# Kernel tuning notes

Hardware: AMD Instinct MI355X
Metric: run time of the kernel (lower is better)

## Reference

```python
import jax, jax.numpy as jnp
import numpy as np

SR = 22050
FMIN = 220.0
N_BINS = 84
BPO = 12
HOP = 512
NORM_P = 1
T_SAMPLES = 8388608  # 2**23 samples of audio


def _make_kernels():
    Q = 1.0 / (2.0 ** (1.0 / BPO) - 1.0)
    fftLen = 2 ** int(np.ceil(np.log2(np.ceil(Q * SR / FMIN))))  # 2048
    freqs = FMIN * 2.0 ** (np.arange(N_BINS) / float(BPO))
    temp = np.zeros((N_BINS, fftLen), dtype=np.complex64)
    for k in range(N_BINS):
        freq = freqs[k]
        l = np.ceil(Q * SR / freq)
        if l % 2 == 1:
            start = int(np.ceil(fftLen / 2.0 - l / 2.0)) - 1
        else:
            start = int(np.ceil(fftLen / 2.0 - l / 2.0))
        li = int(l)
        n = np.arange(li)
        hann = 0.5 - 0.5 * np.cos(2 * np.pi * n / li)  # periodic ('fftbins=True') hann
        idx = np.arange(np.floor(-l / 2.0), np.floor(l / 2.0))
        temp[k, start:start + li] = hann * np.exp(1j * 2 * np.pi * freq / SR * idx) / li
    spec = np.fft.fft(temp, axis=1)[:, : fftLen // 2 + 1]
    kr = spec.real.astype(np.float32)
    ki = spec.imag.astype(np.float32)
    # norm=1 branch: divide by L1 norm (over bins axis, dim=0) of complex magnitude
    mag = np.sqrt(kr ** 2 + ki ** 2)
    denom = np.sum(np.abs(mag), axis=0)  # shape [freq_bins]
    kr = (kr / denom).astype(np.float32)
    ki = (ki / denom).astype(np.float32)
    # Fourier kernels: freq_scale='no', windowing='no'
    freq_bins = fftLen // 2 + 1
    s = np.arange(fftLen, dtype=np.float64)
    kk = np.arange(freq_bins, dtype=np.float64)
    ang = 2 * np.pi * np.outer(kk, s) / fftLen  # [freq_bins, fftLen]
    wsin = np.sin(ang).astype(np.float32)
    wcos = np.cos(ang).astype(np.float32)
    return kr, ki, wcos, wsin


def setup_inputs() -> dict:
    key = jax.random.key(0)
    x = jax.random.normal(key, (T_SAMPLES,), dtype=jnp.float32)
    kr, ki, wcos, wsin = _make_kernels()
    return {
        "x": x,
        "wcos": jnp.asarray(wcos),
        "wsin": jnp.asarray(wsin),
        "kr": jnp.asarray(kr),
        "ki": jnp.asarray(ki),
    }


def reference(x, wcos, wsin, kr, ki):
    fftLen = wcos.shape[1]  # 2048
    n_frames = (x.shape[0] - fftLen) // HOP + 1  # static under jit
    # frame the signal: equivalent to conv1d(x, w, stride=HOP) with kernels w
    idx = jnp.arange(n_frames)[:, None] * HOP + jnp.arange(fftLen)[None, :]
    frames = x[idx]  # [n_frames, fftLen]
    fourier_real = jnp.einsum("fn,kn->kf", frames, wcos)  # [freq_bins, n_frames]
    fourier_imag = jnp.einsum("fn,kn->kf", frames, wsin)
    cqt_real = kr @ fourier_real - ki @ fourier_imag  # [n_bins, n_frames]
    cqt_imag = kr @ fourier_imag + ki @ fourier_real
    cqt = jnp.sqrt(cqt_real ** 2 + cqt_imag ** 2)
    return cqt[None]  # [1, n_bins, n_frames]
```

## Files before the change

### kernel.cpp

```cpp
#include <hip/hip_runtime.h>


#define HOPS 512
#define NBINS 84
#define FREQB 1025
#define NFRAMES 16381
#define TSAMP 8388608
#define SPAN 34304
#define XLSZ 34572
#define KP16 138

typedef short bf16x8 __attribute__((ext_vector_type(8)));
typedef float f32x16 __attribute__((ext_vector_type(16)));

union B8 { struct { ushort4 lo, hi; } p; bf16x8 v; uint4 u; };

__device__ __forceinline__ unsigned short f32_to_bf16(float f) {
    union { float f; unsigned u; } v; v.f = f;
    return (unsigned short)((v.u + 0x7FFFu + ((v.u >> 16) & 1u)) >> 16);
}
__device__ __forceinline__ unsigned pk_bf16(float lo, float hi) {
    return (unsigned)f32_to_bf16(lo) | ((unsigned)f32_to_bf16(hi) << 16);
}
__device__ __forceinline__ bf16x8 pack8(const float* s) {
    B8 r;
    r.u.x = pk_bf16(s[0], s[1]); r.u.y = pk_bf16(s[2], s[3]);
    r.u.z = pk_bf16(s[4], s[5]); r.u.w = pk_bf16(s[6], s[7]);
    return r.v;
}

__device__ __forceinline__ float cos_rev(float r) { return __builtin_amdgcn_cosf(r); }
__device__ __forceinline__ float sin_rev(float r) { return __builtin_amdgcn_sinf(r); }

__global__ __launch_bounds__(64) void aprep_kernel(
    const float* __restrict__ kr, const float* __restrict__ ki,
    unsigned short* __restrict__ Apf)
{
    const int bid = blockIdx.x;
    const int mt = bid / KP16, k16 = bid % KP16;
    const int l = threadIdx.x;
    const int c32 = l & 31, h = l >> 5;
    const int row = mt * 32 + c32;
    const int b = row >> 1, im = row & 1;
    const bool bok = b < NBINS;
    const float* cosp = (im ? ki : kr) + (size_t)(bok ? b : 0) * FREQB;
    const float* sinp = (im ? kr : ki) + (size_t)(bok ? b : 0) * FREQB;
    const float ssign = im ? 1.f : -1.f;

    unsigned short o[8];
    #pragma unroll
    for (int j = 0; j < 8; ++j) {
        int k = k16 * 16 + h * 8 + j;
        float v = 0.f;
        if (bok) {
            if (k <= 1024)       v = cosp[k];
            else if (k <= 2049)  v = ssign * sinp[k - 1025];
        }
        o[j] = f32_to_bf16(v);
    }
    uint4 pk;
    pk.x = (unsigned)o[0] | ((unsigned)o[1] << 16);
    pk.y = (unsigned)o[2] | ((unsigned)o[3] << 16);
    pk.z = (unsigned)o[4] | ((unsigned)o[5] << 16);
    pk.w = (unsigned)o[6] | ((unsigned)o[7] << 16);
    *(uint4*)(Apf + (size_t)bid * 512 + (size_t)l * 8) = pk;
}

__global__ __launch_bounds__(256) void wfused_kernel(
    const unsigned short* __restrict__ Apf, unsigned short* __restrict__ Wpf)
{
    __shared__ float4 red[3][4][64];

    const int bid = blockIdx.x;
    const int mt = bid >> 6, nt = bid & 63;
    const int t = threadIdx.x;
    const int w = t >> 6, l = t & 63;
    const int c32 = l & 31, h = l >> 5;
    const int n = nt * 32 + c32;

    f32x16 acc;
    #pragma unroll
    for (int i = 0; i < 16; ++i) acc[i] = 0.f;

    const int k0 = w * 33;
    const int kcnt = (w < 3) ? 33 : 30;
    const unsigned short* ap = Apf + (size_t)(mt * KP16 + k0) * 512 + (size_t)l * 8;

    for (int i = 0; i < kcnt; ++i) {
        const int k16 = k0 + i;
        B8 bf; bf.u = *(const uint4*)(ap + (size_t)i * 512);
        float tv[8];
        const int kb = k16 * 16 + h * 8;
        if (k16 <= 63) {
            #pragma unroll
            for (int j = 0; j < 8; ++j) {
                int p = __mul24(kb + j, n) & 2047;
                tv[j] = cos_rev((float)p * (1.f / 2048.f));
            }
        } else if (k16 >= 65 && k16 <= 127) {
            #pragma unroll
            for (int j = 0; j < 8; ++j) {
                int p = __mul24(kb + j - 1025, n) & 2047;
                tv[j] = sin_rev((float)p * (1.f / 2048.f));
            }
        } else {
            #pragma unroll
            for (int j = 0; j < 8; ++j) {
                int k = kb + j;
                float v = 0.f;
                if (k <= 1024) {
                    int p = __mul24(k, n) & 2047;
                    v = cos_rev((float)p * (1.f / 2048.f));
                } else if (k <= 2049) {
                    int p = __mul24(k - 1025, n) & 2047;
                    v = sin_rev((float)p * (1.f / 2048.f));
                }
                tv[j] = v;
            }
        }
        acc = __builtin_amdgcn_mfma_f32_32x32x16_bf16(pack8(tv), bf.v, acc, 0, 0, 0);
    }

    if (w > 0) {
        #pragma unroll
        for (int q = 0; q < 4; ++q)
            red[w - 1][q][l] = make_float4(acc[4*q+0], acc[4*q+1], acc[4*q+2], acc[4*q+3]);
    }
    __syncthreads();
    if (w == 0) {
        #pragma unroll
        for (int s = 0; s < 3; ++s) {
            #pragma unroll
            for (int q = 0; q < 4; ++q) {
                float4 v = red[s][q][l];
                acc[4*q+0] += v.x; acc[4*q+1] += v.y;
                acc[4*q+2] += v.z; acc[4*q+3] += v.w;
            }
        }
        #pragma unroll
        for (int g = 0; g < 4; ++g) {
            uint2 qo;
            qo.x = pk_bf16(acc[4*g+0], acc[4*g+1]);
            qo.y = pk_bf16(acc[4*g+2], acc[4*g+3]);
            size_t off = (size_t)(mt * 128 + nt * 2 + (g >> 1)) * 512
                       + (size_t)(c32 + 32 * (g & 1)) * 8 + 4 * h;
            *(uint2*)(Wpf + off) = qo;
        }
    }
}

__global__ __launch_bounds__(768) void cqt_kernel(
    const float* __restrict__ x, const unsigned short* __restrict__ Wpf,
    float* __restrict__ out)
{
    __shared__ __align__(16) unsigned short xl[XLSZ];

    const int t = threadIdx.x;
    const int f0 = blockIdx.x * 64;
    const long S0 = (long)f0 * HOPS;
    const int valid = (int)((TSAMP - S0) < (long)SPAN ? (TSAMP - S0) : (long)SPAN);

    #pragma unroll
    for (int i = 0; i < 12; ++i) {
        int idx4 = t + i * 768;
        if (idx4 < 8576) {
            int s = idx4 * 4;
            float4 v = make_float4(0.f, 0.f, 0.f, 0.f);
            if (s + 4 <= valid) v = *(const float4*)(x + S0 + s);
            ushort4 o;
            o.x = f32_to_bf16(v.x); o.y = f32_to_bf16(v.y);
            o.z = f32_to_bf16(v.z); o.w = f32_to_bf16(v.w);
            *(ushort4*)(&xl[s + 4 * (s >> 9)]) = o;
        }
    }
    __syncthreads();

    const int w = t >> 6, l = t & 63;
    const int mg = w >> 1, fg = w & 1;
    const int c32 = l & 31, h = l >> 5;

    const unsigned short* apf = Wpf + (size_t)mg * (128 * 512) + l * 8;
    const int sbase = (fg * 32 + c32) * HOPS + h * 8;

    f32x16 acc;
    #pragma unroll
    for (int i = 0; i < 16; ++i) acc[i] = 0.f;

    auto ldsB = [&](int k16) -> bf16x8 {
        int s = sbase + k16 * 16;
        int off = s + 4 * (s >> 9);
        B8 r;
        r.p.lo = *(const ushort4*)(&xl[off]);
        r.p.hi = *(const ushort4*)(&xl[off + 4]);
        return r.v;
    };

    uint4 Abuf[2][8];
    #pragma unroll
    for (int j = 0; j < 8; ++j)
        Abuf[0][j] = *(const uint4*)(apf + (size_t)j * 512);

    #pragma unroll
    for (int c = 0; c < 16; ++c) {
        const int cur = c & 1, nxt = cur ^ 1;
        if (c < 15) {
            #pragma unroll
            for (int j = 0; j < 8; ++j)
                Abuf[nxt][j] = *(const uint4*)(apf + (size_t)((c + 1) * 8 + j) * 512);
        }
        #pragma unroll
        for (int j = 0; j < 8; ++j) {
            B8 af; af.u = Abuf[cur][j];
            acc = __builtin_amdgcn_mfma_f32_32x32x16_bf16(af.v, ldsB(c * 8 + j), acc, 0, 0, 0);
        }
    }

    const int f = f0 + fg * 32 + c32;
    if (f < NFRAMES) {
        #pragma unroll
        for (int rp = 0; rp < 4; ++rp) {
            int base = mg * 32 + 8 * rp + 4 * h;
            int b0 = base >> 1;
            float r0 = acc[4 * rp + 0], i0 = acc[4 * rp + 1];
            float r1 = acc[4 * rp + 2], i1 = acc[4 * rp + 3];
            if (b0 < NBINS)
                out[(size_t)b0 * NFRAMES + f] = sqrtf(r0 * r0 + i0 * i0);
            if (b0 + 1 < NBINS)
                out[(size_t)(b0 + 1) * NFRAMES + f] = sqrtf(r1 * r1 + i1 * i1);
        }
    }
}

extern "C" void kernel_launch(void* const* d_in, const int* in_sizes, int n_in,
                              void* d_out, int out_size, void* d_ws, size_t ws_size,
                              hipStream_t stream) {
    const float* x    = (const float*)d_in[0];
    const float* kr   = (const float*)d_in[3];
    const float* ki   = (const float*)d_in[4];
    float* out = (float*)d_out;

    unsigned short* Wpf = (unsigned short*)d_ws;
    unsigned short* Apf = (unsigned short*)((char*)d_ws + 786432);

    aprep_kernel<<<dim3(6 * KP16), dim3(64), 0, stream>>>(kr, ki, Apf);
    wfused_kernel<<<dim3(384), dim3(256), 0, stream>>>(Apf, Wpf);
    cqt_kernel<<<dim3(256), dim3(768), 0, stream>>>(x, Wpf, out);
}
```

Baseline: 118.2 us.

## Halve cqt block tile to 32 frames, raise occupancy, add nontemporal IO and setprio

The cqt kernel now gives each block 32 frames and 6 waves (one per M-tile) instead of 64 frames and 12 waves. This doubles the grid to 512 blocks so all CUs get work, and halves LDS per block so 3 blocks can share a CU. Input loads and output stores become nontemporal, and the MFMA loop runs at raised wave priority. In exchange, each block re-stages more overlapping audio per frame, and every block reads the full W matrix, doubling total W traffic from L2.

New measurement: 124.4 us. 5.2% more time.

```diff
diff --git a/kernel.cpp b/kernel.cpp
--- a/kernel.cpp
+++ b/kernel.cpp
@@ -6,12 +6,13 @@
 #define FREQB 1025
 #define NFRAMES 16381
 #define TSAMP 8388608
-#define SPAN 34304
-#define XLSZ 34572
+#define SPAN32 17920
+#define XL32 18060
 #define KP16 138
 
 typedef short bf16x8 __attribute__((ext_vector_type(8)));
 typedef float f32x16 __attribute__((ext_vector_type(16)));
+typedef float f32x4 __attribute__((ext_vector_type(4)));
 
 union B8 { struct { ushort4 lo, hi; } p; bf16x8 v; uint4 u; };
 
@@ -149,24 +150,25 @@
     }
 }
 
-__global__ __launch_bounds__(768) void cqt_kernel(
+__global__ __launch_bounds__(384, 3) void cqt_kernel(
     const float* __restrict__ x, const unsigned short* __restrict__ Wpf,
     float* __restrict__ out)
 {
-    __shared__ __align__(16) unsigned short xl[XLSZ];
+    __shared__ __align__(16) unsigned short xl[XL32];
 
     const int t = threadIdx.x;
-    const int f0 = blockIdx.x * 64;
+    const int f0 = blockIdx.x * 32;
     const long S0 = (long)f0 * HOPS;
-    const int valid = (int)((TSAMP - S0) < (long)SPAN ? (TSAMP - S0) : (long)SPAN);
+    const int valid = (int)((TSAMP - S0) < (long)SPAN32 ? (TSAMP - S0) : (long)SPAN32);
 
     #pragma unroll
     for (int i = 0; i < 12; ++i) {
-        int idx4 = t + i * 768;
-        if (idx4 < 8576) {
+        int idx4 = t + i * 384;
+        if (idx4 < 4480) {
             int s = idx4 * 4;
-            float4 v = make_float4(0.f, 0.f, 0.f, 0.f);
-            if (s + 4 <= valid) v = *(const float4*)(x + S0 + s);
+            f32x4 v = {0.f, 0.f, 0.f, 0.f};
+            if (s + 4 <= valid)
+                v = __builtin_nontemporal_load((const f32x4*)(x + S0 + s));
             ushort4 o;
             o.x = f32_to_bf16(v.x); o.y = f32_to_bf16(v.y);
             o.z = f32_to_bf16(v.z); o.w = f32_to_bf16(v.w);
@@ -176,11 +178,10 @@
     __syncthreads();
 
     const int w = t >> 6, l = t & 63;
-    const int mg = w >> 1, fg = w & 1;
     const int c32 = l & 31, h = l >> 5;
-
-    const unsigned short* apf = Wpf + (size_t)mg * (128 * 512) + l * 8;
-    const int sbase = (fg * 32 + c32) * HOPS + h * 8;
+    const int sbase = c32 * HOPS + h * 8;
+
+    const unsigned short* apf = Wpf + (size_t)w * (128 * 512) + (size_t)l * 8;
 
     f32x16 acc;
     #pragma unroll
@@ -200,6 +201,7 @@
     for (int j = 0; j < 8; ++j)
         Abuf[0][j] = *(const uint4*)(apf + (size_t)j * 512);
 
+    __builtin_amdgcn_s_setprio(1);
     #pragma unroll
     for (int c = 0; c < 16; ++c) {
         const int cur = c & 1, nxt = cur ^ 1;
@@ -214,19 +216,22 @@
             acc = __builtin_amdgcn_mfma_f32_32x32x16_bf16(af.v, ldsB(c * 8 + j), acc, 0, 0, 0);
         }
     }
-
-    const int f = f0 + fg * 32 + c32;
+    __builtin_amdgcn_s_setprio(0);
+
+    const int f = f0 + c32;
     if (f < NFRAMES) {
         #pragma unroll
         for (int rp = 0; rp < 4; ++rp) {
-            int base = mg * 32 + 8 * rp + 4 * h;
+            int base = w * 32 + 8 * rp + 4 * h;
             int b0 = base >> 1;
             float r0 = acc[4 * rp + 0], i0 = acc[4 * rp + 1];
             float r1 = acc[4 * rp + 2], i1 = acc[4 * rp + 3];
             if (b0 < NBINS)
-                out[(size_t)b0 * NFRAMES + f] = sqrtf(r0 * r0 + i0 * i0);
+                __builtin_nontemporal_store(sqrtf(r0 * r0 + i0 * i0),
+                                            &out[(size_t)b0 * NFRAMES + f]);
             if (b0 + 1 < NBINS)
-                out[(size_t)(b0 + 1) * NFRAMES + f] = sqrtf(r1 * r1 + i1 * i1);
+                __builtin_nontemporal_store(sqrtf(r1 * r1 + i1 * i1),
+                                            &out[(size_t)(b0 + 1) * NFRAMES + f]);
         }
     }
 }
@@ -244,5 +249,5 @@
 
     aprep_kernel<<<dim3(6 * KP16), dim3(64), 0, stream>>>(kr, ki, Apf);
     wfused_kernel<<<dim3(384), dim3(256), 0, stream>>>(Apf, Wpf);
-    cqt_kernel<<<dim3(256), dim3(768), 0, stream>>>(x, Wpf, out);
-}
+    cqt_kernel<<<dim3(512), dim3(384), 0, stream>>>(x, Wpf, out);
+}
```

## Fuse kernel-matrix prep into weight GEMM and XOR-swizzle LDS signal buffer

Applied to the files above, without the earlier changes.

Removes the separate aprep launch by having the weight-building GEMM read kr/ki directly, converting them to bf16 in registers. This saves one kernel launch and the round trip through the Apf workspace, but now does strided fp32 global loads inside the MFMA loop. The cqt kernel also replaces its padded LDS layout with an XOR swizzle, so each B fragment can be read with one 16-byte LDS load instead of two 8-byte loads while still avoiding bank conflicts.

After: 159.4 us. +34.8%, slower.

```diff
diff --git a/kernel.cpp b/kernel.cpp
--- a/kernel.cpp
+++ b/kernel.cpp
@@ -7,8 +7,6 @@
 #define NFRAMES 16381
 #define TSAMP 8388608
 #define SPAN 34304
-#define XLSZ 34572
-#define KP16 138
 
 typedef short bf16x8 __attribute__((ext_vector_type(8)));
 typedef float f32x16 __attribute__((ext_vector_type(16)));
@@ -32,14 +30,19 @@
 __device__ __forceinline__ float cos_rev(float r) { return __builtin_amdgcn_cosf(r); }
 __device__ __forceinline__ float sin_rev(float r) { return __builtin_amdgcn_sinf(r); }
 
-__global__ __launch_bounds__(64) void aprep_kernel(
+__global__ __launch_bounds__(256) void wfused_kernel(
     const float* __restrict__ kr, const float* __restrict__ ki,
-    unsigned short* __restrict__ Apf)
+    unsigned short* __restrict__ Wpf)
 {
+    __shared__ float4 red[3][4][64];
+
     const int bid = blockIdx.x;
-    const int mt = bid / KP16, k16 = bid % KP16;
-    const int l = threadIdx.x;
+    const int mt = bid >> 6, nt = bid & 63;
+    const int t = threadIdx.x;
+    const int w = t >> 6, l = t & 63;
     const int c32 = l & 31, h = l >> 5;
+    const int n = nt * 32 + c32;
+
     const int row = mt * 32 + c32;
     const int b = row >> 1, im = row & 1;
     const bool bok = b < NBINS;
@@ -47,78 +50,50 @@
     const float* sinp = (im ? kr : ki) + (size_t)(bok ? b : 0) * FREQB;
     const float ssign = im ? 1.f : -1.f;
 
-    unsigned short o[8];
-    #pragma unroll
-    for (int j = 0; j < 8; ++j) {
-        int k = k16 * 16 + h * 8 + j;
-        float v = 0.f;
-        if (bok) {
-            if (k <= 1024)       v = cosp[k];
-            else if (k <= 2049)  v = ssign * sinp[k - 1025];
-        }
-        o[j] = f32_to_bf16(v);
-    }
-    uint4 pk;
-    pk.x = (unsigned)o[0] | ((unsigned)o[1] << 16);
-    pk.y = (unsigned)o[2] | ((unsigned)o[3] << 16);
-    pk.z = (unsigned)o[4] | ((unsigned)o[5] << 16);
-    pk.w = (unsigned)o[6] | ((unsigned)o[7] << 16);
-    *(uint4*)(Apf + (size_t)bid * 512 + (size_t)l * 8) = pk;
-}
-
-__global__ __launch_bounds__(256) void wfused_kernel(
-    const unsigned short* __restrict__ Apf, unsigned short* __restrict__ Wpf)
-{
-    __shared__ float4 red[3][4][64];
-
-    const int bid = blockIdx.x;
-    const int mt = bid >> 6, nt = bid & 63;
-    const int t = threadIdx.x;
-    const int w = t >> 6, l = t & 63;
-    const int c32 = l & 31, h = l >> 5;
-    const int n = nt * 32 + c32;
-
     f32x16 acc;
     #pragma unroll
     for (int i = 0; i < 16; ++i) acc[i] = 0.f;
 
     const int k0 = w * 33;
     const int kcnt = (w < 3) ? 33 : 30;
-    const unsigned short* ap = Apf + (size_t)(mt * KP16 + k0) * 512 + (size_t)l * 8;
 
     for (int i = 0; i < kcnt; ++i) {
         const int k16 = k0 + i;
-        B8 bf; bf.u = *(const uint4*)(ap + (size_t)i * 512);
-        float tv[8];
         const int kb = k16 * 16 + h * 8;
+        float tv[8], av[8];
         if (k16 <= 63) {
             #pragma unroll
             for (int j = 0; j < 8; ++j) {
                 int p = __mul24(kb + j, n) & 2047;
                 tv[j] = cos_rev((float)p * (1.f / 2048.f));
+                av[j] = bok ? cosp[kb + j] : 0.f;
             }
         } else if (k16 >= 65 && k16 <= 127) {
+            const int mb = kb - 1025;
             #pragma unroll
             for (int j = 0; j < 8; ++j) {
-                int p = __mul24(kb + j - 1025, n) & 2047;
+                int p = __mul24(mb + j, n) & 2047;
                 tv[j] = sin_rev((float)p * (1.f / 2048.f));
+                av[j] = bok ? ssign * sinp[mb + j] : 0.f;
             }
         } else {
             #pragma unroll
             for (int j = 0; j < 8; ++j) {
                 int k = kb + j;
-                float v = 0.f;
+                float tvv = 0.f, avv = 0.f;
                 if (k <= 1024) {
                     int p = __mul24(k, n) & 2047;
-                    v = cos_rev((float)p * (1.f / 2048.f));
+                    tvv = cos_rev((float)p * (1.f / 2048.f));
+                    avv = bok ? cosp[k] : 0.f;
                 } else if (k <= 2049) {
                     int p = __mul24(k - 1025, n) & 2047;
-                    v = sin_rev((float)p * (1.f / 2048.f));
+                    tvv = sin_rev((float)p * (1.f / 2048.f));
+                    avv = bok ? ssign * sinp[k - 1025] : 0.f;
                 }
-                tv[j] = v;
-            }
-        }
-        acc = __builtin_amdgcn_mfma_f32_32x32x16_bf16(pack8(tv), bf.v, acc, 0, 0, 0);
+                tv[j] = tvv; av[j] = avv;
+            }
+        }
+        acc = __builtin_amdgcn_mfma_f32_32x32x16_bf16(pack8(tv), pack8(av), acc, 0, 0, 0);
     }
 
     if (w > 0) {
@@ -153,7 +128,7 @@
     const float* __restrict__ x, const unsigned short* __restrict__ Wpf,
     float* __restrict__ out)
 {
-    __shared__ __align__(16) unsigned short xl[XLSZ];
+    __shared__ __align__(16) unsigned short xl[SPAN];
 
     const int t = threadIdx.x;
     const int f0 = blockIdx.x * 64;
@@ -170,7 +145,9 @@
             ushort4 o;
             o.x = f32_to_bf16(v.x); o.y = f32_to_bf16(v.y);
             o.z = f32_to_bf16(v.z); o.w = f32_to_bf16(v.w);
-            *(ushort4*)(&xl[s + 4 * (s >> 9)]) = o;
+            int byte = idx4 * 8;
+            int bsw = byte ^ (((byte >> 10) & 7) << 4);
+            *(ushort4*)((char*)xl + bsw) = o;
         }
     }
     __syncthreads();
@@ -179,19 +156,18 @@
     const int mg = w >> 1, fg = w & 1;
     const int c32 = l & 31, h = l >> 5;
 
-    const unsigned short* apf = Wpf + (size_t)mg * (128 * 512) + l * 8;
-    const int sbase = (fg * 32 + c32) * HOPS + h * 8;
+    const unsigned short* apf = Wpf + (size_t)mg * (128 * 512) + (size_t)l * 8;
+    const int byteBase = (fg * 32 + c32) * 1024 + h * 16;
 
     f32x16 acc;
     #pragma unroll
     for (int i = 0; i < 16; ++i) acc[i] = 0.f;
 
     auto ldsB = [&](int k16) -> bf16x8 {
-        int s = sbase + k16 * 16;
-        int off = s + 4 * (s >> 9);
+        int byte = byteBase + k16 * 32;
+        int bsw = byte ^ (((byte >> 10) & 7) << 4);
         B8 r;
-        r.p.lo = *(const ushort4*)(&xl[off]);
-        r.p.hi = *(const ushort4*)(&xl[off + 4]);
+        r.u = *(const uint4*)((const char*)xl + bsw);
         return r.v;
     };
 
@@ -240,9 +216,7 @@
     float* out = (float*)d_out;
 
     unsigned short* Wpf = (unsigned short*)d_ws;
-    unsigned short* Apf = (unsigned short*)((char*)d_ws + 786432);
-
-    aprep_kernel<<<dim3(6 * KP16), dim3(64), 0, stream>>>(kr, ki, Apf);
-    wfused_kernel<<<dim3(384), dim3(256), 0, stream>>>(Apf, Wpf);
+
+    wfused_kernel<<<dim3(384), dim3(256), 0, stream>>>(kr, ki, Wpf);
     cqt_kernel<<<dim3(256), dim3(768), 0, stream>>>(x, Wpf, out);
 }
```
